# Kernel tuning notes

Measured on AMD Instinct MI355X. Metric: run time of the kernel, lower is better.

Reference implementation:

```python
import jax, jax.numpy as jnp
import numpy as np

TEMPERATURE = 0.2


def setup_inputs() -> dict:
    key = jax.random.key(0)
    k1, k2 = jax.random.split(key)
    B, D = 4096, 256
    emb_i = jax.random.normal(k1, (B, D), dtype=jnp.float32)
    emb_j = jax.random.normal(k2, (B, D), dtype=jnp.float32)
    return {"emb_i": emb_i, "emb_j": emb_j}


def _nt_xent(emb_i, emb_j, temperature):
    B = emb_i.shape[0]
    # L2-normalize each embedding (F.normalize, dim=1)
    z_i = emb_i / jnp.linalg.norm(emb_i, axis=1, keepdims=True)
    z_j = emb_j / jnp.linalg.norm(emb_j, axis=1, keepdims=True)
    z = jnp.concatenate([z_i, z_j], axis=0)  # [2B, D], unit rows
    # cosine similarity of unit vectors == dot product: single GEMM instead of
    # the O(N^2 D) broadcasted intermediate in the torch source
    sim = z @ z.T  # [2B, 2B]
    # positives: diag(sim, +B) and diag(sim, -B)
    sim_ij = jnp.einsum('bd,bd->b', z_i, z_j)  # == diag(sim, B)
    positives = jnp.concatenate([sim_ij, sim_ij], axis=0)  # [2B]
    exp_sim = jnp.exp(sim / temperature)
    # mask out self-similarity on the main diagonal
    denom = jnp.sum(exp_sim, axis=1) - jnp.diagonal(exp_sim)
    loss_partial = -(positives / temperature - jnp.log(denom))
    return jnp.sum(loss_partial) / (2 * B)


def reference(emb_i, emb_j):
    return _nt_xent(emb_i, emb_j, TEMPERATURE)
```

## Files before the change

kernel.cpp:

```cpp
#include <hip/hip_runtime.h>
#include <hip/hip_bf16.h>

#define D_DIM 256
#define TEMP 0.2f
#define ZSCALE 2.6857913f
#define TGRID 64
#define NBLK 256
#define NTILES 2080

typedef float f32x4 __attribute__((ext_vector_type(4)));

typedef const __attribute__((address_space(1))) void* gptr_t;
typedef __attribute__((address_space(3))) void* lptr_t;

__global__ __launch_bounds__(256) void nt_normalize(
    const float* __restrict__ ei, const float* __restrict__ ej,
    unsigned char* __restrict__ z8, float* __restrict__ pos, int B) {
  int b = blockIdx.x;
  int d = threadIdx.x;
  float xi = ei[(size_t)b * D_DIM + d];
  float xj = ej[(size_t)b * D_DIM + d];
  float si = xi * xi, sj = xj * xj, sij = xi * xj;
  for (int off = 1; off < 64; off <<= 1) {
    si  += __shfl_xor(si, off);
    sj  += __shfl_xor(sj, off);
    sij += __shfl_xor(sij, off);
  }
  __shared__ float red[3][4];
  int wv = threadIdx.x >> 6, lane = threadIdx.x & 63;
  if (lane == 0) { red[0][wv] = si; red[1][wv] = sj; red[2][wv] = sij; }
  __syncthreads();
  si  = red[0][0] + red[0][1] + red[0][2] + red[0][3];
  sj  = red[1][0] + red[1][1] + red[1][2] + red[1][3];
  sij = red[2][0] + red[2][1] + red[2][2] + red[2][3];
  float ri = rsqrtf(si), rj = rsqrtf(sj);
  float zif = xi * ri * ZSCALE;
  float zjf = xj * rj * ZSCALE;
  float zih = __shfl_down(zif, 1);
  float zjh = __shfl_down(zjf, 1);
  if ((d & 1) == 0) {
    int pki = __builtin_amdgcn_cvt_pk_fp8_f32(zif, zih, 0, false);
    int pkj = __builtin_amdgcn_cvt_pk_fp8_f32(zjf, zjh, 0, false);
    ushort* zi_row = (ushort*)(z8 + (size_t)b * D_DIM);
    ushort* zj_row = (ushort*)(z8 + (size_t)(B + b) * D_DIM);
    zi_row[d >> 1] = (ushort)(pki & 0xffff);
    zj_row[d >> 1] = (ushort)(pkj & 0xffff);
  }
  if (threadIdx.x == 0) pos[b] = sij * ri * rj;
}

__global__ __launch_bounds__(512, 2) void nt_gemm_rowsum(
    const unsigned char* __restrict__ z8, float* __restrict__ partial, int N) {
  int hw = blockIdx.x;
  int b = (hw & 7) * (NBLK / 8) + (hw >> 3);
  int s = (b * NTILES) / NBLK;
  int e = ((b + 1) * NTILES) / NBLK;

  int rem = s, rt = 0;
  while (rem >= TGRID - rt) { rem -= TGRID - rt; ++rt; }
  int ct = rt + rem;

  __shared__ __align__(16) unsigned char Bs[2][128 * 256];
  __shared__ float red_r[4][128];
  __shared__ float red_c[4][128];

  int t = threadIdx.x, lane = t & 63, wv = t >> 6;
  int wr = wv >> 2, wc = wv & 3;

  auto STAGE = [&](int buf, int panel) {
    char* dst = (char*)Bs[buf];
#pragma unroll
    for (int p = 0; p < 4; ++p) {
      int chunk = p * 512 + t;
      int row = chunk >> 4;
      int c = chunk & 15;
      int cl = c ^ (row & 7);
      const char* g = (const char*)z8 + (size_t)(panel * 128 + row) * 256 + cl * 16;
      __builtin_amdgcn_global_load_lds((gptr_t)g, (lptr_t)(dst + chunk * 16), 16, 0, 0);
    }
  };

  unsigned long af[8][4];
  auto READ_AF = [&](int buf) {
    const char* src = (const char*)Bs[buf];
#pragma unroll
    for (int ks = 0; ks < 8; ++ks)
#pragma unroll
      for (int m = 0; m < 4; ++m) {
        int r = wr * 64 + m * 16 + (lane & 15);
        int addr = ((r << 8) + ks * 32 + ((lane >> 4) << 3)) ^ ((r & 7) << 4);
        af[ks][m] = *reinterpret_cast<const unsigned long*>(src + addr);
      }
  };

  STAGE(0, rt);
  bool d0 = (ct == rt);
  if (!d0) STAGE(1, ct);
  __syncthreads();
  READ_AF(0);
  __syncthreads();
  int bp = d0 ? 0 : 1;

  for (int idx = s; idx < e; ++idx) {
    bool lastrow = (ct == TGRID - 1);
    bool more = (idx + 1 < e);
    if (more) STAGE(bp ^ 1, lastrow ? (rt + 1) : (ct + 1));

    f32x4 acc[4][2];
#pragma unroll
    for (int m = 0; m < 4; ++m)
#pragma unroll
      for (int n = 0; n < 2; ++n) acc[m][n] = f32x4{0.f, 0.f, 0.f, 0.f};
    const char* cb = (const char*)Bs[bp];
#pragma unroll
    for (int ks = 0; ks < 8; ++ks) {
      unsigned long bfr[2];
#pragma unroll
      for (int n = 0; n < 2; ++n) {
        int r = wc * 32 + n * 16 + (lane & 15);
        int addr = ((r << 8) + ks * 32 + ((lane >> 4) << 3)) ^ ((r & 7) << 4);
        bfr[n] = *reinterpret_cast<const unsigned long*>(cb + addr);
      }
#pragma unroll
      for (int m = 0; m < 4; ++m)
#pragma unroll
        for (int n = 0; n < 2; ++n)
          acc[m][n] = __builtin_amdgcn_mfma_f32_16x16x32_fp8_fp8(
              (long)af[ks][m], (long)bfr[n], acc[m][n], 0, 0, 0);
    }

    bool isdiag = (rt == ct);
    int rbase = rt * 128 + wr * 64;
    int cbase = ct * 128 + wc * 32 + (lane & 15);
#pragma unroll
    for (int m = 0; m < 4; ++m)
#pragma unroll
      for (int n = 0; n < 2; ++n)
#pragma unroll
        for (int j = 0; j < 4; ++j) {
          int rowg = rbase + m * 16 + (lane >> 4) * 4 + j;
          int colg = cbase + n * 16;
          float ex = exp2f(acc[m][n][j]);
          acc[m][n][j] = (isdiag && rowg == colg) ? 0.f : ex;
        }
#pragma unroll
    for (int m = 0; m < 4; ++m)
#pragma unroll
      for (int j = 0; j < 4; ++j) {
        float rs = acc[m][0][j] + acc[m][1][j];
        rs += __shfl_xor(rs, 1);
        rs += __shfl_xor(rs, 2);
        rs += __shfl_xor(rs, 4);
        rs += __shfl_xor(rs, 8);
        if ((lane & 15) == 0)
          red_r[wc][wr * 64 + m * 16 + (lane >> 4) * 4 + j] = rs;
      }
    if (!isdiag) {
#pragma unroll
      for (int n = 0; n < 2; ++n) {
        float cs = 0.f;
#pragma unroll
        for (int m = 0; m < 4; ++m)
#pragma unroll
          for (int j = 0; j < 4; ++j) cs += acc[m][n][j];
        cs += __shfl_xor(cs, 16);
        int g = lane >> 4;
        if ((g & 1) == 0)
          red_c[wr * 2 + (g >> 1)][wc * 32 + n * 16 + (lane & 15)] = cs;
      }
    }
    __syncthreads();

    if (t < 128) {
      float v = red_r[0][t] + red_r[1][t] + red_r[2][t] + red_r[3][t];
      partial[(size_t)ct * N + rt * 128 + t] = v;
    } else if (t < 256 && !isdiag) {
      int c = t - 128;
      float v = red_c[0][c] + red_c[1][c] + red_c[2][c] + red_c[3][c];
      partial[(size_t)rt * N + ct * 128 + c] = v;
    }

    if (more) {
      if (!lastrow) { ++ct; bp ^= 1; }
      else {
        ++rt; ct = rt;
        READ_AF(bp ^ 1);
        bp ^= 1;
      }
    }
    __syncthreads();
  }
}

__global__ __launch_bounds__(256) void nt_rowfinish(
    const float* __restrict__ partial, const float* __restrict__ pos,
    float* __restrict__ blocksum, int N, int B) {
  int r = blockIdx.x * 256 + threadIdx.x;
  float s = 0.f;
#pragma unroll 8
  for (int p = 0; p < 64; ++p) s += partial[(size_t)p * N + r];
  float pv = pos[r < B ? r : r - B];
  float lr = logf(s) - pv * (1.0f / TEMP);
  for (int off = 1; off < 64; off <<= 1) lr += __shfl_xor(lr, off);
  __shared__ float red[4];
  int wv = threadIdx.x >> 6, lane = threadIdx.x & 63;
  if (lane == 0) red[wv] = lr;
  __syncthreads();
  if (threadIdx.x == 0)
    blocksum[blockIdx.x] = red[0] + red[1] + red[2] + red[3];
}

__global__ __launch_bounds__(64) void nt_final(
    const float* __restrict__ blocksum, float* __restrict__ out, int N) {
  int lane = threadIdx.x;
  float s = (lane < 32) ? blocksum[lane] : 0.f;
  for (int off = 1; off < 32; off <<= 1) s += __shfl_xor(s, off);
  if (lane == 0) out[0] = s / (float)N;
}

extern "C" void kernel_launch(void* const* d_in, const int* in_sizes, int n_in,
                              void* d_out, int out_size, void* d_ws, size_t ws_size,
                              hipStream_t stream) {
  const float* ei = (const float*)d_in[0];
  const float* ej = (const float*)d_in[1];
  int B = in_sizes[0] / D_DIM;
  int N = 2 * B;

  char* ws = (char*)d_ws;
  unsigned char* z8 = (unsigned char*)ws;
  float* partial  = (float*)(ws + (size_t)N * D_DIM);
  float* pos      = (float*)(ws + (size_t)N * D_DIM + (size_t)64 * N * 4);
  float* blocksum = pos + B;
  float* out = (float*)d_out;

  nt_normalize<<<B, 256, 0, stream>>>(ei, ej, z8, pos, B);
  nt_gemm_rowsum<<<NBLK, 512, 0, stream>>>(z8, partial, N);
  nt_rowfinish<<<N / 256, 256, 0, stream>>>(partial, pos, blocksum, N, B);
  nt_final<<<1, 64, 0, stream>>>(blocksum, out, N);
}
```

Measured before the change: 64.90 us.

## Read B fragments directly from global, drop LDS reductions, widen partial sums

The GEMM kernel no longer double-buffers the column panel in LDS. Each wave loads its B fragments straight from global/L2, and only the row panel A is staged in LDS when the row changes. Per-wave row and column partial sums are written directly to a four-times-wider partial buffer, which removes the LDS reduction arrays and the per-tile barriers. Cutting LDS use lets the block count and occupancy double (512 blocks, 4 per CU), at the cost of more global traffic, unpipelined global loads inside the MFMA loop, and a larger reduction in the finish kernel.

New measurement: 105.9 us. +63.2%, slower.

```diff
diff --git a/kernel.cpp b/kernel.cpp
--- a/kernel.cpp
+++ b/kernel.cpp
@@ -5,10 +5,11 @@
 #define TEMP 0.2f
 #define ZSCALE 2.6857913f
 #define TGRID 64
-#define NBLK 256
+#define NBLK 512
 #define NTILES 2080
 
 typedef float f32x4 __attribute__((ext_vector_type(4)));
+typedef unsigned long ulong_t;
 
 typedef const __attribute__((address_space(1))) void* gptr_t;
 typedef __attribute__((address_space(3))) void* lptr_t;
@@ -49,7 +50,7 @@
   if (threadIdx.x == 0) pos[b] = sij * ri * rj;
 }
 
-__global__ __launch_bounds__(512, 2) void nt_gemm_rowsum(
+__global__ __launch_bounds__(512, 4) void nt_gemm_rowsum(
     const unsigned char* __restrict__ z8, float* __restrict__ partial, int N) {
   int hw = blockIdx.x;
   int b = (hw & 7) * (NBLK / 8) + (hw >> 3);
@@ -60,73 +61,67 @@
   while (rem >= TGRID - rt) { rem -= TGRID - rt; ++rt; }
   int ct = rt + rem;
 
-  __shared__ __align__(16) unsigned char Bs[2][128 * 256];
-  __shared__ float red_r[4][128];
-  __shared__ float red_c[4][128];
+  __shared__ __align__(16) unsigned char As[128 * 256];
 
   int t = threadIdx.x, lane = t & 63, wv = t >> 6;
   int wr = wv >> 2, wc = wv & 3;
-
-  auto STAGE = [&](int buf, int panel) {
-    char* dst = (char*)Bs[buf];
+  int g = lane >> 4;
+
+  auto STAGE = [&](int panel) {
 #pragma unroll
     for (int p = 0; p < 4; ++p) {
       int chunk = p * 512 + t;
       int row = chunk >> 4;
       int c = chunk & 15;
       int cl = c ^ (row & 7);
-      const char* g = (const char*)z8 + (size_t)(panel * 128 + row) * 256 + cl * 16;
-      __builtin_amdgcn_global_load_lds((gptr_t)g, (lptr_t)(dst + chunk * 16), 16, 0, 0);
+      const char* gsrc = (const char*)z8 + (size_t)(panel * 128 + row) * 256 + cl * 16;
+      __builtin_amdgcn_global_load_lds((gptr_t)gsrc, (lptr_t)((char*)As + chunk * 16), 16, 0, 0);
     }
   };
 
-  unsigned long af[8][4];
-  auto READ_AF = [&](int buf) {
-    const char* src = (const char*)Bs[buf];
+  ulong_t af[8][4];
+  auto READ_AF = [&]() {
 #pragma unroll
     for (int ks = 0; ks < 8; ++ks)
 #pragma unroll
       for (int m = 0; m < 4; ++m) {
         int r = wr * 64 + m * 16 + (lane & 15);
-        int addr = ((r << 8) + ks * 32 + ((lane >> 4) << 3)) ^ ((r & 7) << 4);
-        af[ks][m] = *reinterpret_cast<const unsigned long*>(src + addr);
+        int addr = ((r << 8) + ks * 32 + (g << 3)) ^ ((r & 7) << 4);
+        af[ks][m] = *reinterpret_cast<const ulong_t*>((const char*)As + addr);
       }
   };
 
-  STAGE(0, rt);
-  bool d0 = (ct == rt);
-  if (!d0) STAGE(1, ct);
-  __syncthreads();
-  READ_AF(0);
-  __syncthreads();
-  int bp = d0 ? 0 : 1;
+  int cur_rt = -1;
 
   for (int idx = s; idx < e; ++idx) {
-    bool lastrow = (ct == TGRID - 1);
-    bool more = (idx + 1 < e);
-    if (more) STAGE(bp ^ 1, lastrow ? (rt + 1) : (ct + 1));
+    if (rt != cur_rt) {
+      __syncthreads();
+      STAGE(rt);
+      __syncthreads();
+      READ_AF();
+      cur_rt = rt;
+    }
+
+    const unsigned char* b0 =
+        z8 + (((size_t)(ct * 128 + wc * 32 + (lane & 15))) << 8) + (g << 3);
+    const unsigned char* b1 = b0 + (16 << 8);
 
     f32x4 acc[4][2];
 #pragma unroll
     for (int m = 0; m < 4; ++m)
 #pragma unroll
       for (int n = 0; n < 2; ++n) acc[m][n] = f32x4{0.f, 0.f, 0.f, 0.f};
-    const char* cb = (const char*)Bs[bp];
 #pragma unroll
     for (int ks = 0; ks < 8; ++ks) {
-      unsigned long bfr[2];
-#pragma unroll
-      for (int n = 0; n < 2; ++n) {
-        int r = wc * 32 + n * 16 + (lane & 15);
-        int addr = ((r << 8) + ks * 32 + ((lane >> 4) << 3)) ^ ((r & 7) << 4);
-        bfr[n] = *reinterpret_cast<const unsigned long*>(cb + addr);
-      }
-#pragma unroll
-      for (int m = 0; m < 4; ++m)
-#pragma unroll
-        for (int n = 0; n < 2; ++n)
-          acc[m][n] = __builtin_amdgcn_mfma_f32_16x16x32_fp8_fp8(
-              (long)af[ks][m], (long)bfr[n], acc[m][n], 0, 0, 0);
+      ulong_t bf0 = *reinterpret_cast<const ulong_t*>(b0 + ks * 32);
+      ulong_t bf1 = *reinterpret_cast<const ulong_t*>(b1 + ks * 32);
+#pragma unroll
+      for (int m = 0; m < 4; ++m) {
+        acc[m][0] = __builtin_amdgcn_mfma_f32_16x16x32_fp8_fp8(
+            (long)af[ks][m], (long)bf0, acc[m][0], 0, 0, 0);
+        acc[m][1] = __builtin_amdgcn_mfma_f32_16x16x32_fp8_fp8(
+            (long)af[ks][m], (long)bf1, acc[m][1], 0, 0, 0);
+      }
     }
 
     bool isdiag = (rt == ct);
@@ -138,7 +133,7 @@
       for (int n = 0; n < 2; ++n)
 #pragma unroll
         for (int j = 0; j < 4; ++j) {
-          int rowg = rbase + m * 16 + (lane >> 4) * 4 + j;
+          int rowg = rbase + m * 16 + g * 4 + j;
           int colg = cbase + n * 16;
           float ex = exp2f(acc[m][n][j]);
           acc[m][n][j] = (isdiag && rowg == colg) ? 0.f : ex;
@@ -152,8 +147,10 @@
         rs += __shfl_xor(rs, 2);
         rs += __shfl_xor(rs, 4);
         rs += __shfl_xor(rs, 8);
-        if ((lane & 15) == 0)
-          red_r[wc][wr * 64 + m * 16 + (lane >> 4) * 4 + j] = rs;
+        if ((lane & 15) == 0) {
+          int rowg = rbase + m * 16 + g * 4 + j;
+          partial[(size_t)(4 * ct + wc) * N + rowg] = rs;
+        }
       }
     if (!isdiag) {
 #pragma unroll
@@ -164,31 +161,16 @@
 #pragma unroll
           for (int j = 0; j < 4; ++j) cs += acc[m][n][j];
         cs += __shfl_xor(cs, 16);
-        int g = lane >> 4;
-        if ((g & 1) == 0)
-          red_c[wr * 2 + (g >> 1)][wc * 32 + n * 16 + (lane & 15)] = cs;
-      }
-    }
-    __syncthreads();
-
-    if (t < 128) {
-      float v = red_r[0][t] + red_r[1][t] + red_r[2][t] + red_r[3][t];
-      partial[(size_t)ct * N + rt * 128 + t] = v;
-    } else if (t < 256 && !isdiag) {
-      int c = t - 128;
-      float v = red_c[0][c] + red_c[1][c] + red_c[2][c] + red_c[3][c];
-      partial[(size_t)rt * N + ct * 128 + c] = v;
-    }
-
-    if (more) {
-      if (!lastrow) { ++ct; bp ^= 1; }
-      else {
-        ++rt; ct = rt;
-        READ_AF(bp ^ 1);
-        bp ^= 1;
-      }
-    }
-    __syncthreads();
+        if ((g & 1) == 0) {
+          int colg = cbase + n * 16;
+          int slot = 4 * rt + 2 * wr + (g >> 1);
+          partial[(size_t)slot * N + colg] = cs;
+        }
+      }
+    }
+
+    ++ct;
+    if (ct == TGRID) { ++rt; ct = rt; }
   }
 }
 
@@ -196,9 +178,15 @@
     const float* __restrict__ partial, const float* __restrict__ pos,
     float* __restrict__ blocksum, int N, int B) {
   int r = blockIdx.x * 256 + threadIdx.x;
-  float s = 0.f;
-#pragma unroll 8
-  for (int p = 0; p < 64; ++p) s += partial[(size_t)p * N + r];
+  float s0 = 0.f, s1 = 0.f, s2 = 0.f, s3 = 0.f;
+#pragma unroll 4
+  for (int p = 0; p < 256; p += 4) {
+    s0 += partial[(size_t)p * N + r];
+    s1 += partial[(size_t)(p + 1) * N + r];
+    s2 += partial[(size_t)(p + 2) * N + r];
+    s3 += partial[(size_t)(p + 3) * N + r];
+  }
+  float s = (s0 + s1) + (s2 + s3);
   float pv = pos[r < B ? r : r - B];
   float lr = logf(s) - pv * (1.0f / TEMP);
   for (int off = 1; off < 64; off <<= 1) lr += __shfl_xor(lr, off);
@@ -229,7 +217,7 @@
   char* ws = (char*)d_ws;
   unsigned char* z8 = (unsigned char*)ws;
   float* partial  = (float*)(ws + (size_t)N * D_DIM);
-  float* pos      = (float*)(ws + (size_t)N * D_DIM + (size_t)64 * N * 4);
+  float* pos      = (float*)(ws + (size_t)N * D_DIM + (size_t)256 * N * 4);
   float* blocksum = pos + B;
   float* out = (float*)d_out;
 
```
